# Performance work log

Measured on AMD Instinct MI355X. Metric: run time of the kernel, lower is better.

The kernel has to match this reference:

```python
import jax, jax.numpy as jnp
import numpy as np

DMIN, DMAX = -1.0, 1.0
B, I, O, K = 1024, 256, 256, 128

def setup_inputs() -> dict:
    key = jax.random.key(0)
    k1, k2, k3 = jax.random.split(key, 3)
    x = jax.random.normal(k1, (B, I), dtype=jnp.float32)
    bound = 1.0 / np.sqrt(I)
    base_weight = jax.random.uniform(k2, (O, I), dtype=jnp.float32, minval=-bound, maxval=bound)
    coeff = 0.03 * jax.random.normal(k3, (O, I, K), dtype=jnp.float32)
    coeff = coeff - coeff.mean(axis=-1, keepdims=True)
    return {
        'x': x,
        'base_weight': base_weight,
        'spline_coefficients': coeff,
        'spline_scale': jnp.ones((O, I), dtype=jnp.float32),
        'bias': jnp.zeros((O,), dtype=jnp.float32),
    }


def reference(x, base_weight, spline_coefficients, spline_scale, bias):
    num_knots = spline_coefficients.shape[-1]
    step = (DMAX - DMIN) / (num_knots - 1)
    # input activation (tanh) then clamp to spline domain
    p = jnp.tanh(x)                                   # (B, I)
    c = jnp.clip(p, DMIN, DMAX)
    scaled = (c - DMIN) / step                        # in [0, K-1]
    left = jnp.clip(jnp.floor(scaled).astype(jnp.int32), 0, num_knots - 1)
    right = jnp.minimum(left + 1, num_knots - 1)
    frac = scaled - left.astype(p.dtype)              # (B, I)
    # fold spline_scale into coefficients, then gather only the 2 relevant knots
    Cs = spline_coefficients * spline_scale[..., None]  # (O, I, K)
    ii = jnp.arange(x.shape[1])[None, :]                # (1, I) broadcasts with (B, I)
    cl = Cs[:, ii, left]                                # (O, B, I)
    cr = Cs[:, ii, right]                               # (O, B, I)
    spline = jnp.einsum('bi,obi->bo', 1.0 - frac, cl) + jnp.einsum('bi,obi->bo', frac, cr)
    base = jax.nn.silu(p) @ base_weight.T               # (B, O)
    return base + spline + bias[None, :]
```

## Files before the change

### kernel.cpp

```cpp
#include <hip/hip_runtime.h>

constexpr int Bb = 1024;
constexpr int Ii = 256;
constexpr int Oo = 256;
constexpr int Kk = 128;
constexpr int NCH = 8;

typedef unsigned short u16;
typedef unsigned int u32;
typedef u16 ushort8v __attribute__((ext_vector_type(8)));
typedef float f4v __attribute__((ext_vector_type(4)));

__device__ __forceinline__ float bf16u_to_f(u16 u) {
    union { u32 ui; float f; } c;
    c.ui = ((u32)u) << 16;
    return c.f;
}
__device__ __forceinline__ u16 f_to_bf16(float f) {
    union { float f; u32 u; } c; c.f = f;
    u32 r = c.u + 0x7fffu + ((c.u >> 16) & 1u);
    return (u16)(r >> 16);
}

__global__ __launch_bounds__(256) void kperm(const float* __restrict__ cs,
                                             const float* __restrict__ scale,
                                             const float* __restrict__ wbase,
                                             u16* __restrict__ cp,
                                             u16* __restrict__ wt) {
    __shared__ u16 T[128 * 66];
    int blk = blockIdx.x;
    int chunk = blk & 7;
    int sub = blk >> 3;
    int i  = chunk * 32 + (sub & 31);
    int oh = (sub >> 5) & 1, kh = (sub >> 6) & 1;
    int o0 = oh << 7, kb = kh << 6;
    int t = threadIdx.x;

    {
        int c4 = t & 15;
        int rb = t >> 4;
        const f4v* cs4 = (const f4v*)cs;
#pragma unroll
        for (int p = 0; p < 8; ++p) {
            int r = p * 16 + rb;
            int o = o0 + r;
            float sc = scale[o * Ii + i];
            f4v val = __builtin_nontemporal_load(
                &cs4[(size_t)(o * Ii + i) * (Kk / 4) + kh * 16 + c4]);
            int kl = c4 * 4;
            T[r * 66 + kl + 0] = f_to_bf16(val.x * sc);
            T[r * 66 + kl + 1] = f_to_bf16(val.y * sc);
            T[r * 66 + kl + 2] = f_to_bf16(val.z * sc);
            T[r * 66 + kl + 3] = f_to_bf16(val.w * sc);
        }
    }
    __syncthreads();
    {
        int og = t & 63;
        int kg = t >> 6;
#pragma unroll
        for (int m = 0; m < 16; ++m) {
            int kl = kg * 16 + m;
            u32 lo = T[(og * 2) * 66 + kl];
            u32 hi = T[(og * 2 + 1) * 66 + kl];
            *(u32*)&cp[((size_t)i * Kk + kb + kl) * Oo + o0 + og * 2] = lo | (hi << 16);
        }
    }
    if (blk < 256) {
        int gid = blk * 256 + t;
        wt[gid] = f_to_bf16(
            __builtin_nontemporal_load(&wbase[(gid & 255) * Ii + (gid >> 8)]));
    }
}

__global__ __launch_bounds__(256, 8) void kmain(const float* __restrict__ x,
                                                const char* __restrict__ cpb,
                                                const u16* __restrict__ wt,
                                                float4* __restrict__ part4) {
    __shared__ float4 sf[256];
    __shared__ u16 wbuf[32 * 256];
    int t = threadIdx.x;
    int blk = blockIdx.x;
    int chunk = blk & (NCH - 1);
    int b0 = (blk >> 3) << 3;
    int i0 = chunk << 5;

    {
        int il = t & 31, bl = t >> 5;
        float xv = __builtin_nontemporal_load(
            &x[(size_t)(b0 + bl) * Ii + i0 + il]);
        float e2 = __expf(2.f * xv);
        float p = 1.f - 2.f / (e2 + 1.f);
        float s = p / (1.f + __expf(-p));
        float c = fminf(fmaxf(p, -1.f), 1.f);
        float scaled = (c + 1.f) * ((float)(Kk - 1) * 0.5f);
        int l = (int)floorf(scaled);
        l = min(max(l, 0), Kk - 1);
        int rr = min(l + 1, Kk - 1);
        float4 v;
        v.x = scaled - (float)l;
        v.y = s;
        v.z = __int_as_float(l * (Oo * 2));
        v.w = __int_as_float(rr * (Oo * 2));
        sf[bl * 32 + il] = v;
    }
    {
        const ushort8v* wsrc = (const ushort8v*)(wt + (size_t)i0 * Oo);
        ushort8v* wdst = (ushort8v*)wbuf;
#pragma unroll
        for (int p = 0; p < 4; ++p)
            wdst[t + p * 256] = wsrc[t + p * 256];
    }
    __syncthreads();

    int oq = t & 31;
    int bl = t >> 5;
    float a0=0.f,a1=0.f,a2=0.f,a3=0.f,a4=0.f,a5=0.f,a6=0.f,a7=0.f;
    const char* cbase = cpb + (size_t)i0 * (Kk * Oo * 2) + oq * 16;

#pragma unroll 2
    for (int m = 0; m < 32; ++m) {
        float4 v = sf[bl * 32 + m];
        ushort8v wv = *(const ushort8v*)&wbuf[m * 256 + oq * 8];
        const char* ci = cbase + (size_t)m * (Kk * Oo * 2);
        ushort8v cl = *(const ushort8v*)(ci + __float_as_int(v.z));
        ushort8v cr = *(const ushort8v*)(ci + __float_as_int(v.w));
        float f = v.x, g = 1.f - v.x, s = v.y;
        a0 = fmaf(s, bf16u_to_f(wv[0]), a0); a1 = fmaf(s, bf16u_to_f(wv[1]), a1);
        a2 = fmaf(s, bf16u_to_f(wv[2]), a2); a3 = fmaf(s, bf16u_to_f(wv[3]), a3);
        a4 = fmaf(s, bf16u_to_f(wv[4]), a4); a5 = fmaf(s, bf16u_to_f(wv[5]), a5);
        a6 = fmaf(s, bf16u_to_f(wv[6]), a6); a7 = fmaf(s, bf16u_to_f(wv[7]), a7);
        a0 = fmaf(g, bf16u_to_f(cl[0]), a0); a0 = fmaf(f, bf16u_to_f(cr[0]), a0);
        a1 = fmaf(g, bf16u_to_f(cl[1]), a1); a1 = fmaf(f, bf16u_to_f(cr[1]), a1);
        a2 = fmaf(g, bf16u_to_f(cl[2]), a2); a2 = fmaf(f, bf16u_to_f(cr[2]), a2);
        a3 = fmaf(g, bf16u_to_f(cl[3]), a3); a3 = fmaf(f, bf16u_to_f(cr[3]), a3);
        a4 = fmaf(g, bf16u_to_f(cl[4]), a4); a4 = fmaf(f, bf16u_to_f(cr[4]), a4);
        a5 = fmaf(g, bf16u_to_f(cl[5]), a5); a5 = fmaf(f, bf16u_to_f(cr[5]), a5);
        a6 = fmaf(g, bf16u_to_f(cl[6]), a6); a6 = fmaf(f, bf16u_to_f(cr[6]), a6);
        a7 = fmaf(g, bf16u_to_f(cl[7]), a7); a7 = fmaf(f, bf16u_to_f(cr[7]), a7);
    }

    size_t cstride = (size_t)(Bb * Oo / 4);
    float4 r0; r0.x=a0; r0.y=a1; r0.z=a2; r0.w=a3;
    float4 r1; r1.x=a4; r1.y=a5; r1.z=a6; r1.w=a7;
    size_t pb = (size_t)chunk * cstride + (size_t)(b0 + bl) * (Oo / 4) + oq * 2;
    part4[pb]     = r0;
    part4[pb + 1] = r1;
}

__global__ __launch_bounds__(256) void kreduce(const float4* __restrict__ part4,
                                               const float4* __restrict__ bias4,
                                               float4* __restrict__ out4) {
    int gid = blockIdx.x * 256 + threadIdx.x;
    const f4v* p = (const f4v*)(part4 + gid);
    f4v s = __builtin_nontemporal_load(p);
#pragma unroll
    for (int c = 1; c < NCH; ++c) {
        f4v v = __builtin_nontemporal_load(p + (size_t)c * (Bb * Oo / 4));
        s.x += v.x; s.y += v.y; s.z += v.z; s.w += v.w;
    }
    float4 bv = ((const float4*)bias4)[gid & 63];
    float4 o;
    o.x = s.x + bv.x; o.y = s.y + bv.y; o.z = s.z + bv.z; o.w = s.w + bv.w;
    out4[gid] = o;
}

extern "C" void kernel_launch(void* const* d_in, const int* in_sizes, int n_in,
                              void* d_out, int out_size, void* d_ws, size_t ws_size,
                              hipStream_t stream) {
    const float* x     = (const float*)d_in[0];
    const float* wbase = (const float*)d_in[1];
    const float* coeff = (const float*)d_in[2];
    const float* scale = (const float*)d_in[3];
    const float* bias  = (const float*)d_in[4];
    float* out = (float*)d_out;

    char* ws = (char*)d_ws;
    u16*    cp    = (u16*)ws;
    u16*    wt    = (u16*)(ws + (16u << 20));
    float4* part4 = (float4*)(ws + (17u << 20));

    kperm<<<1024, 256, 0, stream>>>(coeff, scale, wbase, cp, wt);
    kmain<<<1024, 256, 0, stream>>>(x, (const char*)cp, wt, part4);
    kreduce<<<(Bb * Oo / 4) / 256, 256, 0, stream>>>(part4, (const float4*)bias, (float4*)out);
}
```

Measured before the change: 106.2 us.

## Use bf16 dot2 instructions in main loop and store bf16 partial sums

Packs the interpolation weights (1-frac, frac) and the silu value into bf16 pairs and uses v_dot2_f32_bf16 with byte permutes to combine the left and right knot coefficients, which cuts the per-element FMA and conversion count in the inner loop. The partial sums written per input chunk are also stored as bf16 instead of fp32, halving the traffic to and from the workspace in the reduce kernel. The cost is extra rounding: frac, the activations and the partial sums all lose precision, which may affect tolerance.

```diff
diff --git a/kernel.cpp b/kernel.cpp
--- a/kernel.cpp
+++ b/kernel.cpp
@@ -21,6 +21,15 @@
     u32 r = c.u + 0x7fffu + ((c.u >> 16) & 1u);
     return (u16)(r >> 16);
 }
+
+#if __has_builtin(__builtin_amdgcn_fdot2_f32_bf16)
+#define HAS_DOT2 1
+typedef __bf16 bf2 __attribute__((ext_vector_type(2)));
+__device__ __forceinline__ float fdot2bf(u32 ab, u32 cd, float acc) {
+    union { u32 u; bf2 v; } A, B; A.u = ab; B.u = cd;
+    return __builtin_amdgcn_fdot2_f32_bf16(A.v, B.v, acc, false);
+}
+#endif
 
 __global__ __launch_bounds__(256) void kperm(const float* __restrict__ cs,
                                              const float* __restrict__ scale,
@@ -76,7 +85,7 @@
 __global__ __launch_bounds__(256, 8) void kmain(const float* __restrict__ x,
                                                 const char* __restrict__ cpb,
                                                 const u16* __restrict__ wt,
-                                                float4* __restrict__ part4) {
+                                                u16* __restrict__ part) {
     __shared__ float4 sf[256];
     __shared__ u16 wbuf[32 * 256];
     int t = threadIdx.x;
@@ -97,9 +106,11 @@
         int l = (int)floorf(scaled);
         l = min(max(l, 0), Kk - 1);
         int rr = min(l + 1, Kk - 1);
+        float frac = scaled - (float)l;
         float4 v;
-        v.x = scaled - (float)l;
-        v.y = s;
+        v.x = __uint_as_float((u32)f_to_bf16(1.f - frac) |
+                              ((u32)f_to_bf16(frac) << 16));
+        v.y = __uint_as_float((u32)f_to_bf16(s));
         v.z = __int_as_float(l * (Oo * 2));
         v.w = __int_as_float(rr * (Oo * 2));
         sf[bl * 32 + il] = v;
@@ -115,53 +126,75 @@
 
     int oq = t & 31;
     int bl = t >> 5;
-    float a0=0.f,a1=0.f,a2=0.f,a3=0.f,a4=0.f,a5=0.f,a6=0.f,a7=0.f;
+    float a[8] = {0.f,0.f,0.f,0.f,0.f,0.f,0.f,0.f};
     const char* cbase = cpb + (size_t)i0 * (Kk * Oo * 2) + oq * 16;
 
 #pragma unroll 2
     for (int m = 0; m < 32; ++m) {
         float4 v = sf[bl * 32 + m];
-        ushort8v wv = *(const ushort8v*)&wbuf[m * 256 + oq * 8];
+        uint4 wq = *(const uint4*)&wbuf[m * 256 + oq * 8];
         const char* ci = cbase + (size_t)m * (Kk * Oo * 2);
-        ushort8v cl = *(const ushort8v*)(ci + __float_as_int(v.z));
-        ushort8v cr = *(const ushort8v*)(ci + __float_as_int(v.w));
-        float f = v.x, g = 1.f - v.x, s = v.y;
-        a0 = fmaf(s, bf16u_to_f(wv[0]), a0); a1 = fmaf(s, bf16u_to_f(wv[1]), a1);
-        a2 = fmaf(s, bf16u_to_f(wv[2]), a2); a3 = fmaf(s, bf16u_to_f(wv[3]), a3);
-        a4 = fmaf(s, bf16u_to_f(wv[4]), a4); a5 = fmaf(s, bf16u_to_f(wv[5]), a5);
-        a6 = fmaf(s, bf16u_to_f(wv[6]), a6); a7 = fmaf(s, bf16u_to_f(wv[7]), a7);
-        a0 = fmaf(g, bf16u_to_f(cl[0]), a0); a0 = fmaf(f, bf16u_to_f(cr[0]), a0);
-        a1 = fmaf(g, bf16u_to_f(cl[1]), a1); a1 = fmaf(f, bf16u_to_f(cr[1]), a1);
-        a2 = fmaf(g, bf16u_to_f(cl[2]), a2); a2 = fmaf(f, bf16u_to_f(cr[2]), a2);
-        a3 = fmaf(g, bf16u_to_f(cl[3]), a3); a3 = fmaf(f, bf16u_to_f(cr[3]), a3);
-        a4 = fmaf(g, bf16u_to_f(cl[4]), a4); a4 = fmaf(f, bf16u_to_f(cr[4]), a4);
-        a5 = fmaf(g, bf16u_to_f(cl[5]), a5); a5 = fmaf(f, bf16u_to_f(cr[5]), a5);
-        a6 = fmaf(g, bf16u_to_f(cl[6]), a6); a6 = fmaf(f, bf16u_to_f(cr[6]), a6);
-        a7 = fmaf(g, bf16u_to_f(cl[7]), a7); a7 = fmaf(f, bf16u_to_f(cr[7]), a7);
-    }
-
-    size_t cstride = (size_t)(Bb * Oo / 4);
-    float4 r0; r0.x=a0; r0.y=a1; r0.z=a2; r0.w=a3;
-    float4 r1; r1.x=a4; r1.y=a5; r1.z=a6; r1.w=a7;
-    size_t pb = (size_t)chunk * cstride + (size_t)(b0 + bl) * (Oo / 4) + oq * 2;
-    part4[pb]     = r0;
-    part4[pb + 1] = r1;
-}
-
-__global__ __launch_bounds__(256) void kreduce(const float4* __restrict__ part4,
+        uint4 clq = *(const uint4*)(ci + __float_as_int(v.z));
+        uint4 crq = *(const uint4*)(ci + __float_as_int(v.w));
+#ifdef HAS_DOT2
+        u32 gf = __float_as_uint(v.x);
+        u32 se = __float_as_uint(v.y);
+        u32 so = se << 16;
+        u32 cl32[4] = {clq.x, clq.y, clq.z, clq.w};
+        u32 cr32[4] = {crq.x, crq.y, crq.z, crq.w};
+        u32 wv32[4] = {wq.x, wq.y, wq.z, wq.w};
+#pragma unroll
+        for (int jp = 0; jp < 4; ++jp) {
+            u32 pe = __builtin_amdgcn_perm(cr32[jp], cl32[jp], 0x05040100u);
+            u32 po = __builtin_amdgcn_perm(cr32[jp], cl32[jp], 0x07060302u);
+            a[2*jp]   = fdot2bf(gf, pe, a[2*jp]);
+            a[2*jp+1] = fdot2bf(gf, po, a[2*jp+1]);
+            a[2*jp]   = fdot2bf(se, wv32[jp], a[2*jp]);
+            a[2*jp+1] = fdot2bf(so, wv32[jp], a[2*jp+1]);
+        }
+#else
+        u32 gfu = __float_as_uint(v.x);
+        float g = bf16u_to_f((u16)(gfu & 0xffffu));
+        float f = bf16u_to_f((u16)(gfu >> 16));
+        float s = bf16u_to_f((u16)(__float_as_uint(v.y) & 0xffffu));
+        const ushort8v cl = *(const ushort8v*)&clq;
+        const ushort8v cr = *(const ushort8v*)&crq;
+        const ushort8v wv = *(const ushort8v*)&wq;
+#pragma unroll
+        for (int j = 0; j < 8; ++j) {
+            a[j] = fmaf(s, bf16u_to_f(wv[j]), a[j]);
+            a[j] = fmaf(g, bf16u_to_f(cl[j]), a[j]);
+            a[j] = fmaf(f, bf16u_to_f(cr[j]), a[j]);
+        }
+#endif
+    }
+
+    uint4 pk;
+    pk.x = (u32)f_to_bf16(a[0]) | ((u32)f_to_bf16(a[1]) << 16);
+    pk.y = (u32)f_to_bf16(a[2]) | ((u32)f_to_bf16(a[3]) << 16);
+    pk.z = (u32)f_to_bf16(a[4]) | ((u32)f_to_bf16(a[5]) << 16);
+    pk.w = (u32)f_to_bf16(a[6]) | ((u32)f_to_bf16(a[7]) << 16);
+    *(uint4*)&part[(size_t)chunk * (Bb * Oo) + (size_t)(b0 + bl) * Oo + oq * 8] = pk;
+}
+
+__global__ __launch_bounds__(256) void kreduce(const u32* __restrict__ part2,
                                                const float4* __restrict__ bias4,
                                                float4* __restrict__ out4) {
     int gid = blockIdx.x * 256 + threadIdx.x;
-    const f4v* p = (const f4v*)(part4 + gid);
-    f4v s = __builtin_nontemporal_load(p);
-#pragma unroll
-    for (int c = 1; c < NCH; ++c) {
-        f4v v = __builtin_nontemporal_load(p + (size_t)c * (Bb * Oo / 4));
-        s.x += v.x; s.y += v.y; s.z += v.z; s.w += v.w;
-    }
-    float4 bv = ((const float4*)bias4)[gid & 63];
+    const u32* p = part2 + (size_t)gid * 2;
+    float s0 = 0.f, s1 = 0.f, s2 = 0.f, s3 = 0.f;
+#pragma unroll
+    for (int c = 0; c < NCH; ++c) {
+        u32 lo = __builtin_nontemporal_load(p + (size_t)c * (Bb * Oo / 2));
+        u32 hi = __builtin_nontemporal_load(p + (size_t)c * (Bb * Oo / 2) + 1);
+        s0 += bf16u_to_f((u16)(lo & 0xffffu));
+        s1 += bf16u_to_f((u16)(lo >> 16));
+        s2 += bf16u_to_f((u16)(hi & 0xffffu));
+        s3 += bf16u_to_f((u16)(hi >> 16));
+    }
+    float4 bv = bias4[gid & 63];
     float4 o;
-    o.x = s.x + bv.x; o.y = s.y + bv.y; o.z = s.z + bv.z; o.w = s.w + bv.w;
+    o.x = s0 + bv.x; o.y = s1 + bv.y; o.z = s2 + bv.z; o.w = s3 + bv.w;
     out4[gid] = o;
 }
 
@@ -176,11 +209,13 @@
     float* out = (float*)d_out;
 
     char* ws = (char*)d_ws;
-    u16*    cp    = (u16*)ws;
-    u16*    wt    = (u16*)(ws + (16u << 20));
-    float4* part4 = (float4*)(ws + (17u << 20));
+    u16* cp   = (u16*)ws;
+    u16* wt   = (u16*)(ws + (16u << 20));
+    u16* part = (u16*)(ws + (17u << 20));
 
     kperm<<<1024, 256, 0, stream>>>(coeff, scale, wbase, cp, wt);
-    kmain<<<1024, 256, 0, stream>>>(x, (const char*)cp, wt, part4);
-    kreduce<<<(Bb * Oo / 4) / 256, 256, 0, stream>>>(part4, (const float4*)bias, (float4*)out);
-}
+    kmain<<<1024, 256, 0, stream>>>(x, (const char*)cp, wt, part);
+    kreduce<<<(Bb * Oo / 4) / 256, 256, 0, stream>>>((const u32*)part,
+                                                     (const float4*)bias,
+                                                     (float4*)out);
+}
```

New measurement: 107.4 us. About the same (+1.1%).
